# Kernel tuning notes

Measured on AMD Instinct MI355X. Metric: run time of the kernel, lower is better.

Reference implementation:

```python
import jax, jax.numpy as jnp
import numpy as np


def setup_inputs() -> dict:
    key = jax.random.key(0)
    k1, k2, k3 = jax.random.split(key, 3)
    B, L, H = 4, 4096, 1024
    x = jax.random.normal(k1, (B, L, H), dtype=jnp.float32)
    # 0.02 scale keeps attention logits in a sane range (like trained weights)
    in_proj_weight = jax.random.normal(k2, (3 * H, H), dtype=jnp.float32) * 0.02
    in_proj_bias = jnp.zeros((3 * H,), dtype=jnp.float32)
    out_proj_weight = jax.random.normal(k3, (H, H), dtype=jnp.float32) * 0.02
    out_proj_bias = jnp.zeros((H,), dtype=jnp.float32)
    return {
        "x": x,
        "in_proj_weight": in_proj_weight,
        "in_proj_bias": in_proj_bias,
        "out_proj_weight": out_proj_weight,
        "out_proj_bias": out_proj_bias,
        "num_heads": 16,
        "window_size": 128,
    }


def _windowed_mha(x, in_proj_weight, in_proj_bias, out_proj_weight, out_proj_bias,
                  num_heads, window_size):
    B, L, H = x.shape
    P = window_size
    pad = (-L) % P  # static
    xp = jnp.pad(x, ((0, 0), (0, pad), (0, 0))) if pad else x
    Lp = xp.shape[1]
    nw = Lp // P
    w = xp.reshape(B * nw, P, H)  # [NW, P, H]
    # packed QKV projection (torch MHA: q,k,v = split(x @ W_in.T + b_in))
    qkv = jnp.einsum('nph,dh->npd', w, in_proj_weight) + in_proj_bias
    q, k, v = jnp.split(qkv, 3, axis=-1)
    hd = H // num_heads

    def to_heads(t):
        return t.reshape(B * nw, P, num_heads, hd).transpose(0, 2, 1, 3)  # [NW, Hh, P, hd]

    q, k, v = to_heads(q), to_heads(k), to_heads(v)
    scale = 1.0 / jnp.sqrt(jnp.asarray(hd, dtype=x.dtype))
    scores = jnp.einsum('nhqd,nhkd->nhqk', q * scale, k)  # [NW, Hh, P, P]
    attn = jax.nn.softmax(scores, axis=-1)
    o = jnp.einsum('nhqk,nhkd->nhqd', attn, v)  # [NW, Hh, P, hd]
    o = o.transpose(0, 2, 1, 3).reshape(B * nw, P, H)
    o = jnp.einsum('nph,oh->npo', o, out_proj_weight) + out_proj_bias
    o = o.reshape(B, Lp, H)
    return o[:, :L]


def reference(x, in_proj_weight, in_proj_bias, out_proj_weight, out_proj_bias,
              num_heads, window_size):
    return _windowed_mha(x, in_proj_weight, in_proj_bias, out_proj_weight,
                         out_proj_bias, num_heads, window_size)
```

## Files before the change

kernel.cpp:

```cpp
#include <hip/hip_runtime.h>
#include <hip/hip_bf16.h>
#include <cstdint>


typedef __bf16 bf16_t;
typedef __bf16 bf16x8 __attribute__((ext_vector_type(8)));
typedef float  floatx4 __attribute__((ext_vector_type(4)));

#define MFMA_16x16x32(A, B, C) __builtin_amdgcn_mfma_f32_16x16x32_bf16(A, B, C, 0, 0, 0)

__device__ __forceinline__ void gld_lds16(const bf16_t* g, bf16_t* l) {
  __builtin_amdgcn_global_load_lds(
      (__attribute__((address_space(1))) void*)(void*)(g),
      (__attribute__((address_space(3))) void*)(l), 16, 0, 0);
}

__global__ void cvt_f32_to_bf16(const float* __restrict__ src,
                                bf16_t* __restrict__ dst, int n8) {
  int i = blockIdx.x * blockDim.x + threadIdx.x;
  if (i >= n8) return;
  const float4* s4 = (const float4*)src;
  float4 a = s4[2 * (size_t)i];
  float4 b = s4[2 * (size_t)i + 1];
  bf16x8 o;
  o[0] = (bf16_t)a.x; o[1] = (bf16_t)a.y; o[2] = (bf16_t)a.z; o[3] = (bf16_t)a.w;
  o[4] = (bf16_t)b.x; o[5] = (bf16_t)b.y; o[6] = (bf16_t)b.z; o[7] = (bf16_t)b.w;
  *(bf16x8*)(dst + (size_t)i * 8) = o;
}

template <bool F32OUT>
__global__ __launch_bounds__(256, 2) void gemm_bt(
    const bf16_t* __restrict__ A, const bf16_t* __restrict__ Bm,
    const float* __restrict__ bias, void* __restrict__ Cp,
    int M, int N, int K) {
  __shared__ bf16_t As[128 * 32];
  __shared__ bf16_t Bs[128 * 32];
  const int tid  = threadIdx.x;
  const int lane = tid & 63;
  const int wave = tid >> 6;
  const int n16  = lane & 15;
  const int q4   = lane >> 4;
  const int wm   = (wave >> 1) * 64;
  const int wn   = (wave & 1) * 64;
  const int m0   = blockIdx.y * 128;
  const int n0   = blockIdx.x * 128;

  floatx4 acc[4][4] = {};

  for (int k0 = 0; k0 < K; k0 += 32) {
    __syncthreads();
#pragma unroll
    for (int it = 0; it < 2; ++it) {
      const int ch = it * 256 + wave * 64 + lane;
      const int r = ch >> 2, c = (ch & 3) * 8;
      bf16_t* ldsbase = (it == 0) ? nullptr : nullptr;
      gld_lds16(A + (size_t)(m0 + r) * K + k0 + c,
                As + (size_t)(it * 256 + wave * 64) * 8);
      gld_lds16(Bm + (size_t)(n0 + r) * K + k0 + c,
                Bs + (size_t)(it * 256 + wave * 64) * 8);
    }
    __syncthreads();

    bf16x8 af[4], bf[4];
#pragma unroll
    for (int i = 0; i < 4; ++i)
      af[i] = *(const bf16x8*)&As[(wm + i * 16 + n16) * 32 + q4 * 8];
#pragma unroll
    for (int j = 0; j < 4; ++j)
      bf[j] = *(const bf16x8*)&Bs[(wn + j * 16 + n16) * 32 + q4 * 8];
#pragma unroll
    for (int i = 0; i < 4; ++i)
#pragma unroll
      for (int j = 0; j < 4; ++j)
        acc[i][j] = MFMA_16x16x32(af[i], bf[j], acc[i][j]);
  }

#pragma unroll
  for (int i = 0; i < 4; ++i)
#pragma unroll
    for (int j = 0; j < 4; ++j) {
      const int col = n0 + wn + j * 16 + n16;
      const float b = bias[col];
#pragma unroll
      for (int r = 0; r < 4; ++r) {
        const int row = m0 + wm + i * 16 + q4 * 4 + r;
        const float v = acc[i][j][r] + b;
        if (F32OUT)
          ((float*)Cp)[(size_t)row * N + col] = v;
        else
          ((bf16_t*)Cp)[(size_t)row * N + col] = (bf16_t)v;
      }
    }
}

__global__ __launch_bounds__(256, 2) void attn_win(
    const bf16_t* __restrict__ qkv, bf16_t* __restrict__ o) {
  __shared__ bf16_t smem[3 * 128 * 72];
  bf16_t* qs = smem;
  bf16_t* ks_ = smem + 128 * 72;
  bf16_t* vs = smem + 2 * 128 * 72;
  bf16_t* Ps = smem;

  const int wid  = blockIdx.x >> 4;
  const int h    = blockIdx.x & 15;
  const int tid  = threadIdx.x;
  const int lane = tid & 63;
  const int wave = tid >> 6;
  const int n16  = lane & 15;
  const int q4   = lane >> 4;

  const bf16_t* gq = qkv + (size_t)wid * 128 * 3072 + h * 64;
#pragma unroll
  for (int it = 0; it < 4; ++it) {
    const int c = it * 256 + tid;
    const int p = c >> 3, col = (c & 7) * 8;
    const size_t go = (size_t)p * 3072 + col;
    *(bf16x8*)&qs[p * 72 + col]  = *(const bf16x8*)(gq + go);
    *(bf16x8*)&ks_[p * 72 + col] = *(const bf16x8*)(gq + 1024 + go);
    *(bf16x8*)&vs[p * 72 + col]  = *(const bf16x8*)(gq + 2048 + go);
  }
  __syncthreads();

  floatx4 sacc[2][8] = {};
#pragma unroll
  for (int ks = 0; ks < 2; ++ks) {
    bf16x8 aq[2];
#pragma unroll
    for (int i = 0; i < 2; ++i)
      aq[i] = *(const bf16x8*)&qs[(wave * 32 + i * 16 + n16) * 72 + ks * 32 + q4 * 8];
#pragma unroll
    for (int j = 0; j < 8; ++j) {
      bf16x8 bk = *(const bf16x8*)&ks_[(j * 16 + n16) * 72 + ks * 32 + q4 * 8];
      sacc[0][j] = MFMA_16x16x32(aq[0], bk, sacc[0][j]);
      sacc[1][j] = MFMA_16x16x32(aq[1], bk, sacc[1][j]);
    }
  }
  __syncthreads();

  const float scale = 0.125f;
#pragma unroll
  for (int i = 0; i < 2; ++i) {
#pragma unroll
    for (int r = 0; r < 4; ++r) {
      float vals[8];
      float mx = -1e30f;
#pragma unroll
      for (int j = 0; j < 8; ++j) {
        vals[j] = sacc[i][j][r] * scale;
        mx = fmaxf(mx, vals[j]);
      }
      for (int m = 1; m < 16; m <<= 1) mx = fmaxf(mx, __shfl_xor(mx, m, 64));
      float s = 0.f;
#pragma unroll
      for (int j = 0; j < 8; ++j) {
        vals[j] = __expf(vals[j] - mx);
        s += vals[j];
      }
      for (int m = 1; m < 16; m <<= 1) s += __shfl_xor(s, m, 64);
      const float inv = 1.0f / s;
      const int prow = wave * 32 + i * 16 + q4 * 4 + r;
#pragma unroll
      for (int j = 0; j < 8; ++j)
        Ps[prow * 136 + j * 16 + n16] = (bf16_t)(vals[j] * inv);
    }
  }
  __syncthreads();

  floatx4 oacc[2][4] = {};
#pragma unroll
  for (int kk = 0; kk < 4; ++kk) {
    bf16x8 ap[2];
#pragma unroll
    for (int i = 0; i < 2; ++i)
      ap[i] = *(const bf16x8*)&Ps[(wave * 32 + i * 16 + n16) * 136 + kk * 32 + q4 * 8];
#pragma unroll
    for (int j = 0; j < 4; ++j) {
      bf16x8 bv;
#pragma unroll
      for (int t = 0; t < 8; ++t)
        bv[t] = vs[(kk * 32 + q4 * 8 + t) * 72 + j * 16 + n16];
      oacc[0][j] = MFMA_16x16x32(ap[0], bv, oacc[0][j]);
      oacc[1][j] = MFMA_16x16x32(ap[1], bv, oacc[1][j]);
    }
  }

  bf16_t* go = o + (size_t)wid * 128 * 1024 + h * 64;
#pragma unroll
  for (int i = 0; i < 2; ++i)
#pragma unroll
    for (int j = 0; j < 4; ++j)
#pragma unroll
      for (int r = 0; r < 4; ++r) {
        const int row = wave * 32 + i * 16 + q4 * 4 + r;
        go[(size_t)row * 1024 + j * 16 + n16] = (bf16_t)oacc[i][j][r];
      }
}

extern "C" void kernel_launch(void* const* d_in, const int* in_sizes, int n_in,
                              void* d_out, int out_size, void* d_ws, size_t ws_size,
                              hipStream_t stream) {
  const float* x    = (const float*)d_in[0];
  const float* Win  = (const float*)d_in[1];
  const float* bin  = (const float*)d_in[2];
  const float* Wout = (const float*)d_in[3];
  const float* bout = (const float*)d_in[4];
  float* out = (float*)d_out;

  const size_t M = 16384, H = 1024, H3 = 3072;

  bf16_t* xb    = (bf16_t*)d_ws;
  bf16_t* Winb  = xb + M * H;
  bf16_t* Woutb = Winb + H3 * H;
  bf16_t* qkv   = Woutb + H * H;
  bf16_t* ob    = xb;

  cvt_f32_to_bf16<<<dim3((unsigned)(M * H / 8 / 256)), 256, 0, stream>>>(x, xb, (int)(M * H / 8));
  cvt_f32_to_bf16<<<dim3((unsigned)(H3 * H / 8 / 256)), 256, 0, stream>>>(Win, Winb, (int)(H3 * H / 8));
  cvt_f32_to_bf16<<<dim3((unsigned)(H * H / 8 / 256)), 256, 0, stream>>>(Wout, Woutb, (int)(H * H / 8));

  gemm_bt<false><<<dim3((unsigned)(H3 / 128), (unsigned)(M / 128)), 256, 0, stream>>>(
      xb, Winb, bin, qkv, (int)M, (int)H3, (int)H);

  attn_win<<<dim3(2048), 256, 0, stream>>>(qkv, ob);

  gemm_bt<true><<<dim3((unsigned)(H / 128), (unsigned)(M / 128)), 256, 0, stream>>>(
      ob, Woutb, bout, out, (int)M, (int)H, (int)H);
}
```

Before: 344.5 us.

## Fuse QKV projection into windowed attention kernel with per-head repacked weights

The input projection GEMM is merged into the attention kernel. Each block computes the 128x192 Q/K/V slice for one window and head directly from bf16 x and a head-packed copy of W_in, then runs attention from LDS, so the bf16 qkv tensor never goes to HBM. The softmax scale is folded into Q. V is stored transposed in LDS so the PV operand loads become vectorized instead of scalar gathers. Grid order is heads-fastest so blocks share the X window in cache, but the per-block GEMM tile (4x6 accumulators, single-buffered) and the larger LDS footprint may lower occupancy.

```diff
diff --git a/kernel.cpp b/kernel.cpp
--- a/kernel.cpp
+++ b/kernel.cpp
@@ -5,6 +5,7 @@
 
 typedef __bf16 bf16_t;
 typedef __bf16 bf16x8 __attribute__((ext_vector_type(8)));
+typedef __bf16 bf16x4 __attribute__((ext_vector_type(4)));
 typedef float  floatx4 __attribute__((ext_vector_type(4)));
 
 #define MFMA_16x16x32(A, B, C) __builtin_amdgcn_mfma_f32_16x16x32_bf16(A, B, C, 0, 0, 0)
@@ -26,6 +27,23 @@
   o[0] = (bf16_t)a.x; o[1] = (bf16_t)a.y; o[2] = (bf16_t)a.z; o[3] = (bf16_t)a.w;
   o[4] = (bf16_t)b.x; o[5] = (bf16_t)b.y; o[6] = (bf16_t)b.z; o[7] = (bf16_t)b.w;
   *(bf16x8*)(dst + (size_t)i * 8) = o;
+}
+
+__global__ void cvt_repack_win(const float* __restrict__ Win,
+                               bf16_t* __restrict__ Wpk) {
+  const int dr = blockIdx.x;
+  const int head = dr / 192, s = dr - head * 192;
+  const int src = (s < 64) ? head * 64 + s
+                : (s < 128) ? 1024 + head * 64 + (s - 64)
+                            : 2048 + head * 64 + (s - 128);
+  const float4* srow = (const float4*)(Win + (size_t)src * 1024);
+  const int i = threadIdx.x;
+  float4 a = srow[2 * i];
+  float4 b = srow[2 * i + 1];
+  bf16x8 o;
+  o[0] = (bf16_t)a.x; o[1] = (bf16_t)a.y; o[2] = (bf16_t)a.z; o[3] = (bf16_t)a.w;
+  o[4] = (bf16_t)b.x; o[5] = (bf16_t)b.y; o[6] = (bf16_t)b.z; o[7] = (bf16_t)b.w;
+  *(bf16x8*)(Wpk + (size_t)dr * 1024 + i * 8) = o;
 }
 
 template <bool F32OUT>
@@ -53,7 +71,6 @@
     for (int it = 0; it < 2; ++it) {
       const int ch = it * 256 + wave * 64 + lane;
       const int r = ch >> 2, c = (ch & 3) * 8;
-      bf16_t* ldsbase = (it == 0) ? nullptr : nullptr;
       gld_lds16(A + (size_t)(m0 + r) * K + k0 + c,
                 As + (size_t)(it * 256 + wave * 64) * 8);
       gld_lds16(Bm + (size_t)(n0 + r) * K + k0 + c,
@@ -61,18 +78,18 @@
     }
     __syncthreads();
 
-    bf16x8 af[4], bf[4];
+    bf16x8 af[4], bfr[4];
 #pragma unroll
     for (int i = 0; i < 4; ++i)
       af[i] = *(const bf16x8*)&As[(wm + i * 16 + n16) * 32 + q4 * 8];
 #pragma unroll
     for (int j = 0; j < 4; ++j)
-      bf[j] = *(const bf16x8*)&Bs[(wn + j * 16 + n16) * 32 + q4 * 8];
+      bfr[j] = *(const bf16x8*)&Bs[(wn + j * 16 + n16) * 32 + q4 * 8];
 #pragma unroll
     for (int i = 0; i < 4; ++i)
 #pragma unroll
       for (int j = 0; j < 4; ++j)
-        acc[i][j] = MFMA_16x16x32(af[i], bf[j], acc[i][j]);
+        acc[i][j] = MFMA_16x16x32(af[i], bfr[j], acc[i][j]);
   }
 
 #pragma unroll
@@ -93,51 +110,110 @@
     }
 }
 
-__global__ __launch_bounds__(256, 2) void attn_win(
-    const bf16_t* __restrict__ qkv, bf16_t* __restrict__ o) {
-  __shared__ bf16_t smem[3 * 128 * 72];
-  bf16_t* qs = smem;
-  bf16_t* ks_ = smem + 128 * 72;
-  bf16_t* vs = smem + 2 * 128 * 72;
-  bf16_t* Ps = smem;
-
-  const int wid  = blockIdx.x >> 4;
-  const int h    = blockIdx.x & 15;
+__global__ __launch_bounds__(256, 2) void qkv_attn(
+    const bf16_t* __restrict__ X,
+    const bf16_t* __restrict__ Wpk,
+    const float* __restrict__ bin,
+    bf16_t* __restrict__ o)
+{
+  __shared__ bf16_t smem[27136];
+  bf16_t* Xs  = smem;
+  bf16_t* Ws  = smem + 4096;
+  bf16_t* qs  = smem;
+  bf16_t* ks  = smem + 9216;
+  bf16_t* vsT = smem + 18432;
+  bf16_t* Ps  = smem;
+
+  const int h    = blockIdx.x;
+  const int wid  = blockIdx.y;
   const int tid  = threadIdx.x;
   const int lane = tid & 63;
   const int wave = tid >> 6;
   const int n16  = lane & 15;
   const int q4   = lane >> 4;
-
-  const bf16_t* gq = qkv + (size_t)wid * 128 * 3072 + h * 64;
-#pragma unroll
-  for (int it = 0; it < 4; ++it) {
-    const int c = it * 256 + tid;
-    const int p = c >> 3, col = (c & 7) * 8;
-    const size_t go = (size_t)p * 3072 + col;
-    *(bf16x8*)&qs[p * 72 + col]  = *(const bf16x8*)(gq + go);
-    *(bf16x8*)&ks_[p * 72 + col] = *(const bf16x8*)(gq + 1024 + go);
-    *(bf16x8*)&vs[p * 72 + col]  = *(const bf16x8*)(gq + 2048 + go);
+  const int wm   = (wave >> 1) * 64;
+  const int wn   = (wave & 1) * 96;
+
+  const bf16_t* Xg = X + (size_t)wid * 128 * 1024;
+  const bf16_t* Wg = Wpk + (size_t)h * 192 * 1024;
+
+  floatx4 acc[4][6] = {};
+  for (int k0 = 0; k0 < 1024; k0 += 32) {
+    __syncthreads();
+#pragma unroll
+    for (int it = 0; it < 2; ++it) {
+      const int ch = it * 256 + wave * 64 + lane;
+      gld_lds16(Xg + (size_t)(ch >> 2) * 1024 + k0 + (ch & 3) * 8,
+                Xs + (it * 256 + wave * 64) * 8);
+    }
+#pragma unroll
+    for (int it = 0; it < 3; ++it) {
+      const int ch = it * 256 + wave * 64 + lane;
+      gld_lds16(Wg + (size_t)(ch >> 2) * 1024 + k0 + (ch & 3) * 8,
+                Ws + (it * 256 + wave * 64) * 8);
+    }
+    __syncthreads();
+
+    bf16x8 af[4], bfr[6];
+#pragma unroll
+    for (int i = 0; i < 4; ++i)
+      af[i] = *(const bf16x8*)&Xs[(wm + i * 16 + n16) * 32 + q4 * 8];
+#pragma unroll
+    for (int j = 0; j < 6; ++j)
+      bfr[j] = *(const bf16x8*)&Ws[(wn + j * 16 + n16) * 32 + q4 * 8];
+#pragma unroll
+    for (int i = 0; i < 4; ++i)
+#pragma unroll
+      for (int j = 0; j < 6; ++j)
+        acc[i][j] = MFMA_16x16x32(af[i], bfr[j], acc[i][j]);
+  }
+  __syncthreads();
+
+#pragma unroll
+  for (int j = 0; j < 6; ++j) {
+    const int base = wn + j * 16;
+    const int col  = base + n16;
+    const int gb = (base < 64) ? h * 64 + col
+                 : (base < 128) ? 1024 + h * 64 + (col - 64)
+                                : 2048 + h * 64 + (col - 128);
+    const float bias = bin[gb];
+#pragma unroll
+    for (int i = 0; i < 4; ++i) {
+      const int row0 = wm + i * 16 + q4 * 4;
+      if (base < 64) {
+#pragma unroll
+        for (int r = 0; r < 4; ++r)
+          qs[(row0 + r) * 72 + col] = (bf16_t)((acc[i][j][r] + bias) * 0.125f);
+      } else if (base < 128) {
+#pragma unroll
+        for (int r = 0; r < 4; ++r)
+          ks[(row0 + r) * 72 + (col - 64)] = (bf16_t)(acc[i][j][r] + bias);
+      } else {
+        bf16x4 pv;
+#pragma unroll
+        for (int r = 0; r < 4; ++r) pv[r] = (bf16_t)(acc[i][j][r] + bias);
+        *(bf16x4*)&vsT[(col - 128) * 136 + row0] = pv;
+      }
+    }
   }
   __syncthreads();
 
   floatx4 sacc[2][8] = {};
 #pragma unroll
-  for (int ks = 0; ks < 2; ++ks) {
+  for (int ks0 = 0; ks0 < 2; ++ks0) {
     bf16x8 aq[2];
 #pragma unroll
     for (int i = 0; i < 2; ++i)
-      aq[i] = *(const bf16x8*)&qs[(wave * 32 + i * 16 + n16) * 72 + ks * 32 + q4 * 8];
+      aq[i] = *(const bf16x8*)&qs[(wave * 32 + i * 16 + n16) * 72 + ks0 * 32 + q4 * 8];
 #pragma unroll
     for (int j = 0; j < 8; ++j) {
-      bf16x8 bk = *(const bf16x8*)&ks_[(j * 16 + n16) * 72 + ks * 32 + q4 * 8];
+      bf16x8 bk = *(const bf16x8*)&ks[(j * 16 + n16) * 72 + ks0 * 32 + q4 * 8];
       sacc[0][j] = MFMA_16x16x32(aq[0], bk, sacc[0][j]);
       sacc[1][j] = MFMA_16x16x32(aq[1], bk, sacc[1][j]);
     }
   }
   __syncthreads();
 
-  const float scale = 0.125f;
 #pragma unroll
   for (int i = 0; i < 2; ++i) {
 #pragma unroll
@@ -146,7 +222,7 @@
       float mx = -1e30f;
 #pragma unroll
       for (int j = 0; j < 8; ++j) {
-        vals[j] = sacc[i][j][r] * scale;
+        vals[j] = sacc[i][j][r];
         mx = fmaxf(mx, vals[j]);
       }
       for (int m = 1; m < 16; m <<= 1) mx = fmaxf(mx, __shfl_xor(mx, m, 64));
@@ -175,10 +251,7 @@
       ap[i] = *(const bf16x8*)&Ps[(wave * 32 + i * 16 + n16) * 136 + kk * 32 + q4 * 8];
 #pragma unroll
     for (int j = 0; j < 4; ++j) {
-      bf16x8 bv;
-#pragma unroll
-      for (int t = 0; t < 8; ++t)
-        bv[t] = vs[(kk * 32 + q4 * 8 + t) * 72 + j * 16 + n16];
+      bf16x8 bv = *(const bf16x8*)&vsT[(j * 16 + n16) * 136 + kk * 32 + q4 * 8];
       oacc[0][j] = MFMA_16x16x32(ap[0], bv, oacc[0][j]);
       oacc[1][j] = MFMA_16x16x32(ap[1], bv, oacc[1][j]);
     }
@@ -209,19 +282,17 @@
   const size_t M = 16384, H = 1024, H3 = 3072;
 
   bf16_t* xb    = (bf16_t*)d_ws;
-  bf16_t* Winb  = xb + M * H;
-  bf16_t* Woutb = Winb + H3 * H;
-  bf16_t* qkv   = Woutb + H * H;
-  bf16_t* ob    = xb;
-
-  cvt_f32_to_bf16<<<dim3((unsigned)(M * H / 8 / 256)), 256, 0, stream>>>(x, xb, (int)(M * H / 8));
-  cvt_f32_to_bf16<<<dim3((unsigned)(H3 * H / 8 / 256)), 256, 0, stream>>>(Win, Winb, (int)(H3 * H / 8));
-  cvt_f32_to_bf16<<<dim3((unsigned)(H * H / 8 / 256)), 256, 0, stream>>>(Wout, Woutb, (int)(H * H / 8));
-
-  gemm_bt<false><<<dim3((unsigned)(H3 / 128), (unsigned)(M / 128)), 256, 0, stream>>>(
-      xb, Winb, bin, qkv, (int)M, (int)H3, (int)H);
-
-  attn_win<<<dim3(2048), 256, 0, stream>>>(qkv, ob);
+  bf16_t* Wpk   = xb + M * H;
+  bf16_t* Woutb = Wpk + H3 * H;
+  bf16_t* ob    = Woutb + H * H;
+
+  cvt_f32_to_bf16<<<dim3((unsigned)(M * H / 8 / 256)), 256, 0, stream>>>(
+      x, xb, (int)(M * H / 8));
+  cvt_repack_win<<<dim3((unsigned)H3), 128, 0, stream>>>(Win, Wpk);
+  cvt_f32_to_bf16<<<dim3((unsigned)(H * H / 8 / 256)), 256, 0, stream>>>(
+      Wout, Woutb, (int)(H * H / 8));
+
+  qkv_attn<<<dim3(16, 128), 256, 0, stream>>>(xb, Wpk, bin, ob);
 
   gemm_bt<true><<<dim3((unsigned)(H / 128), (unsigned)(M / 128)), 256, 0, stream>>>(
       ob, Woutb, bout, out, (int)M, (int)H, (int)H);
```

Measured after the change: 333.7 us. 3.1% less time.
